# Optimization experiments

Measured on AMD Instinct MI355X. Metric: run time of the kernel, lower is better.

The kernel has to match this reference:

```python
import jax, jax.numpy as jnp
import numpy as np

EMBED_DIM = 1024
NUM_HEADS = 16
HEAD_DIM = EMBED_DIM // NUM_HEADS


def setup_inputs() -> dict:
    key = jax.random.key(0)
    k_x, k_wqkv, k_bqkv, k_wo, k_bo = jax.random.split(key, 5)
    b, n = 2, 2048
    scale_in = 1.0 / np.sqrt(EMBED_DIM)
    return {
        "x": jax.random.normal(k_x, (b, n, EMBED_DIM), dtype=jnp.float32),
        "W_qkv": jax.random.normal(k_wqkv, (EMBED_DIM, 3 * EMBED_DIM), dtype=jnp.float32) * scale_in,
        "b_qkv": jnp.zeros((3 * EMBED_DIM,), dtype=jnp.float32),
        "W_out": jax.random.normal(k_wo, (EMBED_DIM, EMBED_DIM), dtype=jnp.float32) * scale_in,
        "b_out": jnp.zeros((EMBED_DIM,), dtype=jnp.float32),
    }


def _rope_rotate(t, cos, sin):
    # t: [b, h, n, hd]; cos/sin: [1, 1, n, hd//2]
    t1, t2 = jnp.split(t, 2, axis=-1)
    return jnp.concatenate([cos * t1 - sin * t2, sin * t1 + cos * t2], axis=-1)


def reference(x, W_qkv, b_qkv, W_out, b_out):
    b, n, d = x.shape
    h, hd = NUM_HEADS, HEAD_DIM

    qkv = x @ W_qkv + b_qkv                      # [b, n, 3d]
    q, k, v = jnp.split(qkv, 3, axis=-1)
    q, k, v = [t.reshape(b, n, h, hd).transpose(0, 2, 1, 3) for t in (q, k, v)]

    # RoPE tables
    hd2 = hd // 2
    theta = 10000.0 ** (-2.0 * jnp.arange(hd2, dtype=jnp.float32) / hd)
    freqs = jnp.arange(n, dtype=jnp.float32)[:, None] * theta[None, :]  # [n, hd2]
    cos = jnp.cos(freqs)[None, None]
    sin = jnp.sin(freqs)[None, None]
    q = _rope_rotate(q, cos, sin)
    k = _rope_rotate(k, cos, sin)

    scores = jnp.einsum('bhqd,bhkd->bhqk', q, k) / jnp.sqrt(jnp.float32(hd))
    attn = jax.nn.softmax(scores, axis=-1)       # [b, h, n, n]
    out = jnp.einsum('bhqk,bhkd->bhqd', attn, v)
    out = out.transpose(0, 2, 1, 3).reshape(b, n, d)
    return out @ W_out + b_out
```

## Files before the change

### kernel.cpp

```cpp
#include <hip/hip_runtime.h>
#include <hip/hip_bf16.h>
#include <math.h>

#define EMBED 1024
#define NHEAD 16
#define HD 64
#define BATCH 2
#define SEQ 2048
#define MTOT (BATCH * SEQ)
#define QKVN (3 * EMBED)

typedef __attribute__((ext_vector_type(8))) short short8;
typedef __attribute__((ext_vector_type(4))) float f32x4;

typedef __attribute__((address_space(1))) const unsigned int GUI;
typedef __attribute__((address_space(3))) unsigned int LUI;

__device__ __forceinline__ void gload_lds16(const void* src, void* dst) {
  __builtin_amdgcn_global_load_lds((GUI*)src, (LUI*)dst, 16, 0, 0);
}

__device__ __forceinline__ unsigned short f2bf(float f) {
  unsigned u = __builtin_bit_cast(unsigned, f);
  u += 0x7fffu + ((u >> 16) & 1u);
  return (unsigned short)(u >> 16);
}

__device__ __forceinline__ unsigned cvt_pk_bf16(float lo, float hi) {
  unsigned r;
  asm("v_cvt_pk_bf16_f32 %0, %1, %2" : "=v"(r) : "v"(lo), "v"(hi));
  return r;
}

#define QSCALE 0.1803368801111191f


__global__ __launch_bounds__(256) void k_cvt(const float* __restrict__ in,
                                             unsigned short* __restrict__ out, int n4) {
  int i = blockIdx.x * 256 + threadIdx.x;
  if (i >= n4) return;
  float4 v = reinterpret_cast<const float4*>(in)[i];
  ushort4 o;
  o.x = f2bf(v.x); o.y = f2bf(v.y); o.z = f2bf(v.z); o.w = f2bf(v.w);
  reinterpret_cast<ushort4*>(out)[i] = o;
}

__global__ __launch_bounds__(256) void k_transpose_cvt(const float* __restrict__ W,
                                                       unsigned short* __restrict__ WT,
                                                       int K, int Ncols) {
  __shared__ float tile[32][33];
  int n0 = blockIdx.x * 32, k0 = blockIdx.y * 32;
  int tc = threadIdx.x & 31, tr = threadIdx.x >> 5;
  for (int i = 0; i < 4; i++) {
    int r = tr + i * 8;
    tile[r][tc] = W[(size_t)(k0 + r) * Ncols + n0 + tc];
  }
  __syncthreads();
  for (int i = 0; i < 4; i++) {
    int r = tr + i * 8;
    WT[(size_t)(n0 + r) * K + k0 + tc] = f2bf(tile[tc][r]);
  }
}

__global__ __launch_bounds__(256) void k_rope_tables(float* __restrict__ cosT,
                                                     float* __restrict__ sinT) {
  int idx = blockIdx.x * 256 + threadIdx.x;
  if (idx >= SEQ * 32) return;
  int pos = idx >> 5, i = idx & 31;
  float theta = __expf((float)i * -0.28782313662425575f);
  float f = (float)pos * theta;
  cosT[idx] = cosf(f);
  sinT[idx] = sinf(f);
}

__device__ __forceinline__ void gemm_mainloop(const unsigned short* __restrict__ A,
                                              const unsigned short* __restrict__ Bt,
                                              unsigned short* Al, unsigned short* Bl,
                                              size_t m0, size_t n0,
                                              int tid, int l15, int g, int wm, int wn,
                                              f32x4 acc[4][4]) {
  const int w = tid >> 6;
  const int lane = tid & 63;
  const int srow = lane >> 3, slot = lane & 7;
  for (int k0 = 0; k0 < 1024; k0 += 64) {
    __syncthreads();
    for (int it = 0; it < 4; it++) {
      const int r = w * 32 + it * 8 + srow;
      const int sc = (slot ^ (r & 7)) * 8;
      gload_lds16(A + (m0 + r) * 1024 + k0 + sc, &Al[(w * 32 + it * 8) * 64]);
      gload_lds16(Bt + (n0 + r) * 1024 + k0 + sc, &Bl[(w * 32 + it * 8) * 64]);
    }
    __syncthreads();
    for (int kk = 0; kk < 2; kk++) {
      short8 fa[4], fb[4];
      const int xr = ((kk * 4 + g) ^ (l15 & 7)) * 8;
      for (int i = 0; i < 4; i++)
        fa[i] = *reinterpret_cast<const short8*>(&Al[(wm * 64 + i * 16 + l15) * 64 + xr]);
      for (int j = 0; j < 4; j++)
        fb[j] = *reinterpret_cast<const short8*>(&Bl[(wn * 64 + j * 16 + l15) * 64 + xr]);
      for (int i = 0; i < 4; i++)
        for (int j = 0; j < 4; j++)
          acc[i][j] = __builtin_amdgcn_mfma_f32_16x16x32_bf16(fa[i], fb[j], acc[i][j], 0, 0, 0);
    }
  }
}

__global__ __launch_bounds__(256) void k_qkv_gemm(const unsigned short* __restrict__ A,
                                                  const unsigned short* __restrict__ Bt,
                                                  const float* __restrict__ bias,
                                                  const float* __restrict__ cosT,
                                                  const float* __restrict__ sinT,
                                                  unsigned short* __restrict__ Qb,
                                                  unsigned short* __restrict__ Kb,
                                                  unsigned short* __restrict__ Vtg) {
  __shared__ alignas(16) unsigned short Al[128 * 64];
  __shared__ alignas(16) unsigned short Bl[128 * 64];
  const int tid = threadIdx.x;
  const int lane = tid & 63, l15 = lane & 15, g = lane >> 4;
  const int wid = tid >> 6, wm = wid >> 1, wn = wid & 1;
  const size_t m0 = (size_t)blockIdx.y * 128;
  const size_t n0 = (size_t)blockIdx.x * 128;
  f32x4 acc[4][4] = {};
  gemm_mainloop(A, Bt, Al, Bl, m0, n0, tid, l15, g, wm, wn, acc);

  const int cbase = (int)n0 + wn * 64;
  const int sec = cbase >> 10;
  const int head = (cbase & 1023) >> 6;
  float bia[4];
  for (int j = 0; j < 4; j++) bia[j] = bias[cbase + j * 16 + l15];
  const size_t mw = m0 + wm * 64;

  if (sec == 2) {
    for (int i = 0; i < 4; i++) {
      size_t mbase = mw + i * 16 + g * 4;
      int bb = (int)(mbase >> 11), pos0 = (int)(mbase & 2047);
      int k0 = pos0 & 63;
      int col = (pos0 & ~63) | (k0 & 32) | (((k0 >> 2) & 3) << 3) | (((k0 >> 4) & 1) << 2);
      size_t hb = (size_t)(bb * NHEAD + head) * HD;
      for (int j = 0; j < 4; j++) {
        int d = j * 16 + l15;
        uint2 pk;
        pk.x = cvt_pk_bf16(acc[i][j][0] + bia[j], acc[i][j][1] + bia[j]);
        pk.y = cvt_pk_bf16(acc[i][j][2] + bia[j], acc[i][j][3] + bia[j]);
        *reinterpret_cast<uint2*>(Vtg + (hb + d) * SEQ + col) = pk;
      }
    }
  } else {
    unsigned short* dst = sec ? Kb : Qb;
    const float qs = sec ? 1.0f : QSCALE;
    for (int i = 0; i < 4; i++)
      for (int r = 0; r < 4; r++) {
        size_t m = mw + i * 16 + g * 4 + r;
        int bb = (int)(m >> 11), pos = (int)(m & 2047);
        size_t base = ((size_t)(bb * NHEAD + head) * SEQ + pos) * HD;
        const float* cr = cosT + pos * 32;
        const float* sr = sinT + pos * 32;
        for (int pl = 0; pl < 2; pl++) {
          int ii = pl * 16 + l15;
          float c = cr[ii], s = sr[ii];
          float lo = acc[i][pl][r] + bia[pl];
          float hi = acc[i][pl + 2][r] + bia[pl + 2];
          dst[base + ii]      = f2bf((c * lo - s * hi) * qs);
          dst[base + 32 + ii] = f2bf((s * lo + c * hi) * qs);
        }
      }
  }
}

__global__ __launch_bounds__(256) void k_out_gemm(const unsigned short* __restrict__ A,
                                                  const unsigned short* __restrict__ Bt,
                                                  const float* __restrict__ bias,
                                                  float* __restrict__ out) {
  __shared__ alignas(16) unsigned short Al[128 * 64];
  __shared__ alignas(16) unsigned short Bl[64 * 64];
  const int tid = threadIdx.x;
  const int lane = tid & 63, l15 = lane & 15, g = lane >> 4;
  const int wid = tid >> 6, wm = wid >> 1, wn = wid & 1;
  const int w = wid;
  const int srow = lane >> 3, slot = lane & 7;
  const size_t m0 = (size_t)blockIdx.y * 128;
  const size_t n0 = (size_t)blockIdx.x * 64;
  f32x4 acc[4][2] = {};

  for (int k0 = 0; k0 < 1024; k0 += 64) {
    __syncthreads();
    for (int it = 0; it < 4; it++) {
      const int r = w * 32 + it * 8 + srow;
      const int sc = (slot ^ (r & 7)) * 8;
      gload_lds16(A + (m0 + r) * 1024 + k0 + sc, &Al[(w * 32 + it * 8) * 64]);
    }
    for (int it = 0; it < 2; it++) {
      const int r = w * 16 + it * 8 + srow;
      const int sc = (slot ^ (r & 7)) * 8;
      gload_lds16(Bt + (n0 + r) * 1024 + k0 + sc, &Bl[(w * 16 + it * 8) * 64]);
    }
    __syncthreads();
    for (int kk = 0; kk < 2; kk++) {
      short8 fa[4], fb[2];
      const int xr = ((kk * 4 + g) ^ (l15 & 7)) * 8;
      for (int i = 0; i < 4; i++)
        fa[i] = *reinterpret_cast<const short8*>(&Al[(wm * 64 + i * 16 + l15) * 64 + xr]);
      for (int j = 0; j < 2; j++)
        fb[j] = *reinterpret_cast<const short8*>(&Bl[(wn * 32 + j * 16 + l15) * 64 + xr]);
      for (int i = 0; i < 4; i++)
        for (int j = 0; j < 2; j++)
          acc[i][j] = __builtin_amdgcn_mfma_f32_16x16x32_bf16(fa[i], fb[j], acc[i][j], 0, 0, 0);
    }
  }

  const int cbase = (int)n0 + wn * 32;
  const size_t mw = m0 + wm * 64;
  for (int i = 0; i < 4; i++)
    for (int r = 0; r < 4; r++) {
      size_t m = mw + i * 16 + g * 4 + r;
      for (int j = 0; j < 2; j++) {
        int col = cbase + j * 16 + l15;
        out[m * EMBED + col] = acc[i][j][r] + bias[col];
      }
    }
}

__global__ __launch_bounds__(256) void k_attn(const unsigned short* __restrict__ Q,
                                              const unsigned short* __restrict__ Kg,
                                              const unsigned short* __restrict__ Vtg,
                                              float* __restrict__ Opart,
                                              float* __restrict__ lpart) {
  __shared__ alignas(16) unsigned short Kt[64 * 64];
  __shared__ alignas(16) unsigned short Vt[64 * 64];
  const int tid = threadIdx.x, w = tid >> 6, lane = tid & 63;
  const int l15 = lane & 15, g = lane >> 4;
  const int srow = lane >> 3, slot = lane & 7;

  const int n = blockIdx.x;
  const int xcd = n & 7, m = n >> 3;
  const int qb = m & 15, z = m >> 4;
  const int sp = z & 1, bh = (z >> 1) * 8 + xcd;

  const unsigned short* Qp = Q + (size_t)bh * SEQ * HD;
  const unsigned short* Kp = Kg + (size_t)bh * SEQ * HD;
  const unsigned short* Vp = Vtg + (size_t)bh * HD * SEQ;
  const int q0 = qb * 128 + w * 32;

  short8 aq[2][2];
#pragma unroll
  for (int u = 0; u < 2; u++)
#pragma unroll
    for (int kk = 0; kk < 2; kk++)
      aq[u][kk] = *reinterpret_cast<const short8*>(
          Qp + (size_t)(q0 + u * 16 + l15) * HD + kk * 32 + g * 8);

  const int sr16 = w * 16 + srow;
  const int sc0 = (slot ^ (sr16 & 7)) * 8;

  f32x4 o[2][4] = {};
  float lrow[2] = {0.f, 0.f};

  for (int t = sp * 16; t < sp * 16 + 16; t++) {
    const int kb = t * 64;
    __syncthreads();
    gload_lds16(Kp + (size_t)(kb + sr16) * HD + sc0, &Kt[(w * 16) * 64]);
    gload_lds16(Vp + (size_t)sr16 * SEQ + kb + sc0, &Vt[(w * 16) * 64]);
    gload_lds16(Kp + (size_t)(kb + sr16 + 8) * HD + sc0, &Kt[(w * 16 + 8) * 64]);
    gload_lds16(Vp + (size_t)(sr16 + 8) * SEQ + kb + sc0, &Vt[(w * 16 + 8) * 64]);
    __syncthreads();

    f32x4 s[2][4] = {};
#pragma unroll
    for (int kk = 0; kk < 2; kk++) {
      const int xr = ((kk * 4 + g) ^ (l15 & 7)) * 8;
#pragma unroll
      for (int c = 0; c < 4; c++) {
        short8 ak = *reinterpret_cast<const short8*>(&Kt[(c * 16 + l15) * 64 + xr]);
        s[0][c] = __builtin_amdgcn_mfma_f32_16x16x32_bf16(ak, aq[0][kk], s[0][c], 0, 0, 0);
        s[1][c] = __builtin_amdgcn_mfma_f32_16x16x32_bf16(ak, aq[1][kk], s[1][c], 0, 0, 0);
      }
    }

    unsigned wpk[2][8];
#pragma unroll
    for (int u = 0; u < 2; u++) {
      float rs = 0.f;
#pragma unroll
      for (int c = 0; c < 4; c++) {
        float p0 = __builtin_exp2f(s[u][c][0]);
        float p1 = __builtin_exp2f(s[u][c][1]);
        float p2 = __builtin_exp2f(s[u][c][2]);
        float p3 = __builtin_exp2f(s[u][c][3]);
        rs += (p0 + p1) + (p2 + p3);
        wpk[u][2 * c]     = cvt_pk_bf16(p0, p1);
        wpk[u][2 * c + 1] = cvt_pk_bf16(p2, p3);
      }
      lrow[u] += rs;
    }

#pragma unroll
    for (int kk = 0; kk < 2; kk++) {
      const int xr = ((kk * 4 + g) ^ (l15 & 7)) * 8;
      short8 pb0 = __builtin_bit_cast(short8,
          uint4{wpk[0][4 * kk], wpk[0][4 * kk + 1], wpk[0][4 * kk + 2], wpk[0][4 * kk + 3]});
      short8 pb1 = __builtin_bit_cast(short8,
          uint4{wpk[1][4 * kk], wpk[1][4 * kk + 1], wpk[1][4 * kk + 2], wpk[1][4 * kk + 3]});
#pragma unroll
      for (int c2 = 0; c2 < 4; c2++) {
        short8 av = *reinterpret_cast<const short8*>(&Vt[(c2 * 16 + l15) * 64 + xr]);
        o[0][c2] = __builtin_amdgcn_mfma_f32_16x16x32_bf16(av, pb0, o[0][c2], 0, 0, 0);
        o[1][c2] = __builtin_amdgcn_mfma_f32_16x16x32_bf16(av, pb1, o[1][c2], 0, 0, 0);
      }
    }
  }

  const size_t ob = (size_t)(sp * 32 + bh) * HD * SEQ;
#pragma unroll
  for (int u = 0; u < 2; u++) {
    float l = lrow[u];
    l += __shfl_xor(l, 16, 64);
    l += __shfl_xor(l, 32, 64);
    const int pos = q0 + u * 16 + l15;
    if (g == 0) lpart[(size_t)(sp * 32 + bh) * SEQ + pos] = l;
#pragma unroll
    for (int c2 = 0; c2 < 4; c2++)
#pragma unroll
      for (int r = 0; r < 4; r++)
        Opart[ob + (size_t)(c2 * 16 + g * 4 + r) * SEQ + pos] = o[u][c2][r];
  }
}

__global__ __launch_bounds__(256) void k_merge(const float* __restrict__ Op,
                                               const float* __restrict__ lp,
                                               unsigned short* __restrict__ AO) {
  __shared__ float T[64][65];
  __shared__ float Ls[64];
  const int tid = threadIdx.x;
  const int bh = blockIdx.x & 31, pt = blockIdx.x >> 5;
  const int p0 = pt * 64;
  const size_t b0 = (size_t)bh * HD * SEQ;
  const size_t b1 = (size_t)(32 + bh) * HD * SEQ;
  const int pc = tid & 63, dr = tid >> 6;
#pragma unroll
  for (int pass = 0; pass < 16; pass++) {
    const int d = pass * 4 + dr;
    T[d][pc] = Op[b0 + (size_t)d * SEQ + p0 + pc] + Op[b1 + (size_t)d * SEQ + p0 + pc];
  }
  if (tid < 64)
    Ls[tid] = lp[(size_t)bh * SEQ + p0 + tid] + lp[(size_t)(32 + bh) * SEQ + p0 + tid];
  __syncthreads();
  const int pos = tid >> 2, dc = (tid & 3) * 16;
  const float inv = 1.f / Ls[pos];
  const int bb = bh >> 4, h = bh & 15;
  unsigned short* dst = AO + ((size_t)bb * SEQ + p0 + pos) * EMBED + h * HD + dc;
  unsigned pk[8];
#pragma unroll
  for (int i = 0; i < 8; i++)
    pk[i] = cvt_pk_bf16(T[dc + 2 * i][pos] * inv, T[dc + 2 * i + 1][pos] * inv);
  *reinterpret_cast<uint4*>(dst) = uint4{pk[0], pk[1], pk[2], pk[3]};
  *reinterpret_cast<uint4*>(dst + 8) = uint4{pk[4], pk[5], pk[6], pk[7]};
}

extern "C" void kernel_launch(void* const* d_in, const int* in_sizes, int n_in,
                              void* d_out, int out_size, void* d_ws, size_t ws_size,
                              hipStream_t stream) {
  const float* x    = (const float*)d_in[0];
  const float* Wqkv = (const float*)d_in[1];
  const float* bqkv = (const float*)d_in[2];
  const float* Wout = (const float*)d_in[3];
  const float* bout = (const float*)d_in[4];
  float* out = (float*)d_out;

  char* ws = (char*)d_ws;
  size_t off = 0;
  auto carve = [&](size_t bytes) {
    char* p = ws + off;
    off += (bytes + 255) & ~(size_t)255;
    return p;
  };
  float* cosT           = (float*)carve((size_t)SEQ * 32 * 4);
  float* sinT           = (float*)carve((size_t)SEQ * 32 * 4);
  unsigned short* Xb    = (unsigned short*)carve((size_t)MTOT * EMBED * 2);
  unsigned short* WqkvT = (unsigned short*)carve((size_t)QKVN * EMBED * 2);
  unsigned short* WoT   = (unsigned short*)carve((size_t)EMBED * EMBED * 2);
  unsigned short* Qb    = (unsigned short*)carve((size_t)MTOT * EMBED * 2);
  unsigned short* Kb    = (unsigned short*)carve((size_t)MTOT * EMBED * 2);
  unsigned short* Vtg   = (unsigned short*)carve((size_t)MTOT * EMBED * 2);
  unsigned short* AO    = (unsigned short*)carve((size_t)MTOT * EMBED * 2);
  float* Opart          = (float*)carve((size_t)2 * 32 * HD * SEQ * 4);
  float* lpart          = (float*)carve((size_t)2 * 32 * SEQ * 4);

  k_cvt<<<(MTOT * EMBED / 4 + 255) / 256, 256, 0, stream>>>(x, Xb, MTOT * EMBED / 4);
  k_transpose_cvt<<<dim3(QKVN / 32, EMBED / 32), 256, 0, stream>>>(Wqkv, WqkvT, EMBED, QKVN);
  k_transpose_cvt<<<dim3(EMBED / 32, EMBED / 32), 256, 0, stream>>>(Wout, WoT, EMBED, EMBED);
  k_rope_tables<<<(SEQ * 32) / 256, 256, 0, stream>>>(cosT, sinT);

  k_qkv_gemm<<<dim3(QKVN / 128, MTOT / 128), 256, 0, stream>>>(Xb, WqkvT, bqkv, cosT, sinT, Qb, Kb, Vtg);
  k_attn<<<dim3(1024), 256, 0, stream>>>(Qb, Kb, Vtg, Opart, lpart);
  k_merge<<<dim3(1024), 256, 0, stream>>>(Opart, lpart, AO);
  k_out_gemm<<<dim3(EMBED / 64, MTOT / 128), 256, 0, stream>>>(AO, WoT, bout, out);
}
```

Before: 149.4 us.

## Remap GEMM tiles per XCD, shrink attention blocks, row-major partial outputs

The QKV and output GEMMs now use a 1D grid whose block index is remapped so consecutive tiles land on the same XCD, aiming for better L2 reuse of A/B panels. The attention kernel drops to 128 threads with 64-query blocks and twice as many blocks, and each warp now loads 32 K/V rows per tile. The first QK MFMA starts from zero instead of an accumulator, and exp2 uses the hardware builtin. Partial outputs are stored row-major with vector stores, so the merge kernel reads contiguous float4s without an LDS transpose. The risk is that halving the query block doubles K/V traffic per query.

```diff
diff --git a/kernel.cpp b/kernel.cpp
--- a/kernel.cpp
+++ b/kernel.cpp
@@ -31,6 +31,12 @@
   asm("v_cvt_pk_bf16_f32 %0, %1, %2" : "=v"(r) : "v"(lo), "v"(hi));
   return r;
 }
+
+#if __has_builtin(__builtin_amdgcn_exp2f)
+#define EXP2(x) __builtin_amdgcn_exp2f(x)
+#else
+#define EXP2(x) __builtin_exp2f(x)
+#endif
 
 #define QSCALE 0.1803368801111191f
 
@@ -118,8 +124,10 @@
   const int tid = threadIdx.x;
   const int lane = tid & 63, l15 = lane & 15, g = lane >> 4;
   const int wid = tid >> 6, wm = wid >> 1, wn = wid & 1;
-  const size_t m0 = (size_t)blockIdx.y * 128;
-  const size_t n0 = (size_t)blockIdx.x * 128;
+  const int bid = blockIdx.x;
+  const int tile = (bid & 7) * 96 + (bid >> 3);
+  const size_t m0 = (size_t)(tile / 24) * 128;
+  const size_t n0 = (size_t)(tile % 24) * 128;
   f32x4 acc[4][4] = {};
   gemm_mainloop(A, Bt, Al, Bl, m0, n0, tid, l15, g, wm, wn, acc);
 
@@ -178,8 +186,10 @@
   const int wid = tid >> 6, wm = wid >> 1, wn = wid & 1;
   const int w = wid;
   const int srow = lane >> 3, slot = lane & 7;
-  const size_t m0 = (size_t)blockIdx.y * 128;
-  const size_t n0 = (size_t)blockIdx.x * 64;
+  const int bid = blockIdx.x;
+  const int tile = (bid & 7) * 64 + (bid >> 3);
+  const size_t m0 = (size_t)(tile / 16) * 128;
+  const size_t n0 = (size_t)(tile % 16) * 64;
   f32x4 acc[4][2] = {};
 
   for (int k0 = 0; k0 < 1024; k0 += 64) {
@@ -220,7 +230,7 @@
     }
 }
 
-__global__ __launch_bounds__(256) void k_attn(const unsigned short* __restrict__ Q,
+__global__ __launch_bounds__(128) void k_attn(const unsigned short* __restrict__ Q,
                                               const unsigned short* __restrict__ Kg,
                                               const unsigned short* __restrict__ Vtg,
                                               float* __restrict__ Opart,
@@ -233,13 +243,13 @@
 
   const int n = blockIdx.x;
   const int xcd = n & 7, m = n >> 3;
-  const int qb = m & 15, z = m >> 4;
+  const int qb = m & 31, z = m >> 5;
   const int sp = z & 1, bh = (z >> 1) * 8 + xcd;
 
   const unsigned short* Qp = Q + (size_t)bh * SEQ * HD;
   const unsigned short* Kp = Kg + (size_t)bh * SEQ * HD;
   const unsigned short* Vp = Vtg + (size_t)bh * HD * SEQ;
-  const int q0 = qb * 128 + w * 32;
+  const int q0 = qb * 64 + w * 32;
 
   short8 aq[2][2];
 #pragma unroll
@@ -249,30 +259,40 @@
       aq[u][kk] = *reinterpret_cast<const short8*>(
           Qp + (size_t)(q0 + u * 16 + l15) * HD + kk * 32 + g * 8);
 
-  const int sr16 = w * 16 + srow;
-  const int sc0 = (slot ^ (sr16 & 7)) * 8;
-
+  const int kb0 = sp * 1024;
+  const f32x4 z4 = {0.f, 0.f, 0.f, 0.f};
   f32x4 o[2][4] = {};
   float lrow[2] = {0.f, 0.f};
 
-  for (int t = sp * 16; t < sp * 16 + 16; t++) {
-    const int kb = t * 64;
-    __syncthreads();
-    gload_lds16(Kp + (size_t)(kb + sr16) * HD + sc0, &Kt[(w * 16) * 64]);
-    gload_lds16(Vp + (size_t)sr16 * SEQ + kb + sc0, &Vt[(w * 16) * 64]);
-    gload_lds16(Kp + (size_t)(kb + sr16 + 8) * HD + sc0, &Kt[(w * 16 + 8) * 64]);
-    gload_lds16(Vp + (size_t)(sr16 + 8) * SEQ + kb + sc0, &Vt[(w * 16 + 8) * 64]);
-    __syncthreads();
-
-    f32x4 s[2][4] = {};
-#pragma unroll
-    for (int kk = 0; kk < 2; kk++) {
-      const int xr = ((kk * 4 + g) ^ (l15 & 7)) * 8;
+  for (int t = 0; t < 16; t++) {
+    const int kb = kb0 + t * 64;
+    __syncthreads();
+#pragma unroll
+    for (int it = 0; it < 4; it++) {
+      const int r = w * 32 + it * 8 + srow;
+      const int sc = (slot ^ (r & 7)) * 8;
+      gload_lds16(Kp + (size_t)(kb + r) * HD + sc, &Kt[(w * 32 + it * 8) * 64]);
+      gload_lds16(Vp + (size_t)r * SEQ + kb + sc, &Vt[(w * 32 + it * 8) * 64]);
+    }
+    __syncthreads();
+
+    f32x4 s[2][4];
+    {
+      const int xr = (g ^ (l15 & 7)) * 8;
 #pragma unroll
       for (int c = 0; c < 4; c++) {
         short8 ak = *reinterpret_cast<const short8*>(&Kt[(c * 16 + l15) * 64 + xr]);
-        s[0][c] = __builtin_amdgcn_mfma_f32_16x16x32_bf16(ak, aq[0][kk], s[0][c], 0, 0, 0);
-        s[1][c] = __builtin_amdgcn_mfma_f32_16x16x32_bf16(ak, aq[1][kk], s[1][c], 0, 0, 0);
+        s[0][c] = __builtin_amdgcn_mfma_f32_16x16x32_bf16(ak, aq[0][0], z4, 0, 0, 0);
+        s[1][c] = __builtin_amdgcn_mfma_f32_16x16x32_bf16(ak, aq[1][0], z4, 0, 0, 0);
+      }
+    }
+    {
+      const int xr = ((4 + g) ^ (l15 & 7)) * 8;
+#pragma unroll
+      for (int c = 0; c < 4; c++) {
+        short8 ak = *reinterpret_cast<const short8*>(&Kt[(c * 16 + l15) * 64 + xr]);
+        s[0][c] = __builtin_amdgcn_mfma_f32_16x16x32_bf16(ak, aq[0][1], s[0][c], 0, 0, 0);
+        s[1][c] = __builtin_amdgcn_mfma_f32_16x16x32_bf16(ak, aq[1][1], s[1][c], 0, 0, 0);
       }
     }
 
@@ -282,10 +302,10 @@
       float rs = 0.f;
 #pragma unroll
       for (int c = 0; c < 4; c++) {
-        float p0 = __builtin_exp2f(s[u][c][0]);
-        float p1 = __builtin_exp2f(s[u][c][1]);
-        float p2 = __builtin_exp2f(s[u][c][2]);
-        float p3 = __builtin_exp2f(s[u][c][3]);
+        float p0 = EXP2(s[u][c][0]);
+        float p1 = EXP2(s[u][c][1]);
+        float p2 = EXP2(s[u][c][2]);
+        float p3 = EXP2(s[u][c][3]);
         rs += (p0 + p1) + (p2 + p3);
         wpk[u][2 * c]     = cvt_pk_bf16(p0, p1);
         wpk[u][2 * c + 1] = cvt_pk_bf16(p2, p3);
@@ -309,7 +329,7 @@
     }
   }
 
-  const size_t ob = (size_t)(sp * 32 + bh) * HD * SEQ;
+  const size_t ob = (size_t)(sp * 32 + bh) * SEQ * HD;
 #pragma unroll
   for (int u = 0; u < 2; u++) {
     float l = lrow[u];
@@ -317,42 +337,34 @@
     l += __shfl_xor(l, 32, 64);
     const int pos = q0 + u * 16 + l15;
     if (g == 0) lpart[(size_t)(sp * 32 + bh) * SEQ + pos] = l;
+    float* orow = Opart + ob + (size_t)pos * HD;
 #pragma unroll
     for (int c2 = 0; c2 < 4; c2++)
-#pragma unroll
-      for (int r = 0; r < 4; r++)
-        Opart[ob + (size_t)(c2 * 16 + g * 4 + r) * SEQ + pos] = o[u][c2][r];
+      *reinterpret_cast<f32x4*>(orow + c2 * 16 + g * 4) = o[u][c2];
   }
 }
 
 __global__ __launch_bounds__(256) void k_merge(const float* __restrict__ Op,
                                                const float* __restrict__ lp,
                                                unsigned short* __restrict__ AO) {
-  __shared__ float T[64][65];
-  __shared__ float Ls[64];
-  const int tid = threadIdx.x;
-  const int bh = blockIdx.x & 31, pt = blockIdx.x >> 5;
-  const int p0 = pt * 64;
-  const size_t b0 = (size_t)bh * HD * SEQ;
-  const size_t b1 = (size_t)(32 + bh) * HD * SEQ;
-  const int pc = tid & 63, dr = tid >> 6;
-#pragma unroll
-  for (int pass = 0; pass < 16; pass++) {
-    const int d = pass * 4 + dr;
-    T[d][pc] = Op[b0 + (size_t)d * SEQ + p0 + pc] + Op[b1 + (size_t)d * SEQ + p0 + pc];
-  }
-  if (tid < 64)
-    Ls[tid] = lp[(size_t)bh * SEQ + p0 + tid] + lp[(size_t)(32 + bh) * SEQ + p0 + tid];
-  __syncthreads();
-  const int pos = tid >> 2, dc = (tid & 3) * 16;
-  const float inv = 1.f / Ls[pos];
+  const int t = threadIdx.x;
+  const int bh = blockIdx.x >> 5, pt = blockIdx.x & 31;
+  const int pos = pt * 64 + (t >> 2), dc = (t & 3) * 16;
+  const float* p0 = Op + ((size_t)bh * SEQ + pos) * HD + dc;
+  const float* p1 = p0 + (size_t)32 * SEQ * HD;
+  const float l = lp[(size_t)bh * SEQ + pos] + lp[(size_t)(32 + bh) * SEQ + pos];
+  const float inv = 1.f / l;
+  unsigned pk[8];
+#pragma unroll
+  for (int i = 0; i < 4; i++) {
+    float4 a = reinterpret_cast<const float4*>(p0)[i];
+    float4 b = reinterpret_cast<const float4*>(p1)[i];
+    pk[2 * i]     = cvt_pk_bf16((a.x + b.x) * inv, (a.y + b.y) * inv);
+    pk[2 * i + 1] = cvt_pk_bf16((a.z + b.z) * inv, (a.w + b.w) * inv);
+  }
   const int bb = bh >> 4, h = bh & 15;
-  unsigned short* dst = AO + ((size_t)bb * SEQ + p0 + pos) * EMBED + h * HD + dc;
-  unsigned pk[8];
-#pragma unroll
-  for (int i = 0; i < 8; i++)
-    pk[i] = cvt_pk_bf16(T[dc + 2 * i][pos] * inv, T[dc + 2 * i + 1][pos] * inv);
-  *reinterpret_cast<uint4*>(dst) = uint4{pk[0], pk[1], pk[2], pk[3]};
+  unsigned short* dst = AO + ((size_t)bb * SEQ + pos) * EMBED + h * HD + dc;
+  *reinterpret_cast<uint4*>(dst)     = uint4{pk[0], pk[1], pk[2], pk[3]};
   *reinterpret_cast<uint4*>(dst + 8) = uint4{pk[4], pk[5], pk[6], pk[7]};
 }
 
@@ -390,8 +402,8 @@
   k_transpose_cvt<<<dim3(EMBED / 32, EMBED / 32), 256, 0, stream>>>(Wout, WoT, EMBED, EMBED);
   k_rope_tables<<<(SEQ * 32) / 256, 256, 0, stream>>>(cosT, sinT);
 
-  k_qkv_gemm<<<dim3(QKVN / 128, MTOT / 128), 256, 0, stream>>>(Xb, WqkvT, bqkv, cosT, sinT, Qb, Kb, Vtg);
-  k_attn<<<dim3(1024), 256, 0, stream>>>(Qb, Kb, Vtg, Opart, lpart);
+  k_qkv_gemm<<<dim3(768), 256, 0, stream>>>(Xb, WqkvT, bqkv, cosT, sinT, Qb, Kb, Vtg);
+  k_attn<<<dim3(2048), 128, 0, stream>>>(Qb, Kb, Vtg, Opart, lpart);
   k_merge<<<dim3(1024), 256, 0, stream>>>(Opart, lpart, AO);
-  k_out_gemm<<<dim3(EMBED / 64, MTOT / 128), 256, 0, stream>>>(AO, WoT, bout, out);
-}
+  k_out_gemm<<<dim3(512), 256, 0, stream>>>(AO, WoT, bout, out);
+}
```

Measured after the change: 146.0 us. -2.3%, faster.
